# Optimization experiments

Hardware: AMD Instinct MI355X
Metric: run time of the kernel (lower is better)

## Reference

```python
import jax, jax.numpy as jnp
import numpy as np

B, N, F, FS, OUT, S, H, K = 1024, 256, 64, 128, 128, 4, 4, 4
EPS = 1e-5   # BatchNorm1d eps
BIG = 1e9    # sentinel distance for invalid nodes

# fully-connected segment edges (S nodes per graph, B graphs, flat node indexing)
_base = np.array([(i, j) for i in range(S) for j in range(S) if i != j], dtype=np.int32).T
_offs = (np.arange(B, dtype=np.int32) * S)[:, None]
CSRC = jnp.asarray((_base[0][None, :] + _offs).reshape(-1))
CDST = jnp.asarray((_base[1][None, :] + _offs).reshape(-1))
CMASK = jnp.ones(CSRC.shape[0], jnp.float32)


def _bn_relu(h, gamma, beta):
    # BatchNorm1d in training mode: biased batch statistics over the node axis
    mu = h.mean(0)
    var = jnp.var(h, axis=0)
    return jax.nn.relu((h - mu) * jax.lax.rsqrt(var + EPS) * gamma + beta)


def _graph_conv(x, src, dst, emask, W, b, gamma, beta):
    # linear -> gather(src) -> scatter-add(dst) -> degree norm -> BN -> ReLU
    h = x @ W + b
    agg = jax.ops.segment_sum(h[src] * emask[:, None], dst, num_segments=x.shape[0])
    deg = jnp.clip(jax.ops.segment_sum(emask, dst, num_segments=x.shape[0]), 1.0, None)
    return _bn_relu(h + agg / deg[:, None], gamma, beta)


def _knn_edges(positions, presence):
    # edges (i -> j) for each valid node i to its K nearest valid neighbors j
    valid = presence > 0.5                                    # [B,N]
    n_valid = valid.sum(-1)                                   # [B]
    diff = positions[:, :, None, :] - positions[:, None, :, :]
    d2 = jax.lax.stop_gradient(jnp.sum(diff * diff, -1))      # squared dist, same ordering as cdist
    d2 = jnp.where(valid[:, None, :], d2, BIG)                # mask invalid columns
    negv, idx = jax.lax.top_k(-d2, K + 1)                     # nearest first; idx[...,0] is self (dist 0)
    nbr, nd = idx[:, :, 1:], -negv[:, :, 1:]                  # [B,N,K]
    emask = valid[:, :, None] & (n_valid[:, None, None] >= 2) & (nd < 0.5 * BIG)
    offs = (jnp.arange(B) * N)[:, None, None]
    src = jnp.broadcast_to(jnp.arange(N)[None, :, None] + offs, (B, N, K)).reshape(-1)
    dst = jnp.where(emask, nbr + offs, 0).reshape(-1)
    return src, dst, emask.reshape(-1).astype(jnp.float32)


def setup_inputs() -> dict:
    key = jax.random.key(0)
    ks = jax.random.split(key, 16)
    rn = lambda k, shp, s=0.05: jax.random.normal(k, shp, jnp.float32) * s
    return {
        "axle_features": jax.random.normal(ks[0], (B, N, F), jnp.float32),
        "axle_positions": jax.random.normal(ks[1], (B, N, 2), jnp.float32),
        "presence_scores": jax.random.uniform(ks[2], (B, N), jnp.float32),
        "seg_queries": jax.random.normal(ks[3], (S, F), jnp.float32),
        "wq": rn(ks[4], (F, F)), "bq": jnp.zeros((F,), jnp.float32),
        "wk": rn(ks[5], (F, F)), "bk": jnp.zeros((F,), jnp.float32),
        "w_a2s": rn(ks[6], (F, FS)), "b_a2s": jnp.zeros((FS,), jnp.float32),
        "w_s2a": rn(ks[7], (FS, F)), "b_s2a": jnp.zeros((F,), jnp.float32),
        "coarse_W": rn(ks[8], (2, FS, FS)), "coarse_b": jnp.zeros((2, FS), jnp.float32),
        "coarse_gamma": jnp.ones((2, FS), jnp.float32), "coarse_beta": jnp.zeros((2, FS), jnp.float32),
        "fine_W": rn(ks[9], (3, F, F)), "fine_b": jnp.zeros((3, F), jnp.float32),
        "fine_gamma": jnp.ones((3, F), jnp.float32), "fine_beta": jnp.zeros((3, F), jnp.float32),
        "w_out": rn(ks[10], (F, OUT)), "b_out": jnp.zeros((OUT,), jnp.float32),
    }


def reference(axle_features, axle_positions, presence_scores, seg_queries, wq, bq, wk, bk,
              w_a2s, b_a2s, w_s2a, b_s2a, coarse_W, coarse_b, coarse_gamma, coarse_beta,
              fine_W, fine_b, fine_gamma, fine_beta, w_out, b_out):
    hd = F // H
    # LearnableSegmentation: MHA attention weights (head-averaged), then softmax over segments
    q = (seg_queries @ wq + bq).reshape(S, H, hd)
    k = (axle_features @ wk + bk).reshape(B, N, H, hd)
    scores = jnp.einsum('shd,bnhd->bhsn', q, k) / np.sqrt(hd)
    attn = jax.nn.softmax(scores, -1).mean(1)                 # [B,S,N]
    assign = jax.nn.softmax(jnp.swapaxes(attn, 1, 2), -1)     # [B,N,S]
    # segment pooling + coarse GNN over fully-connected segment graph
    proj = axle_features @ w_a2s + b_a2s                      # [B,N,FS]
    sf = jnp.einsum('bns,bnf->bsf', assign, proj).reshape(B * S, FS)
    for l in range(coarse_W.shape[0]):
        sf = _graph_conv(sf, CSRC, CDST, CMASK, coarse_W[l], coarse_b[l], coarse_gamma[l], coarse_beta[l])
    ctx = jnp.einsum('bns,bsf->bnf', assign, sf.reshape(B, S, FS)) @ w_s2a + b_s2a
    # fine GNN over kNN axle graph
    src, dst, em = _knn_edges(axle_positions, presence_scores)
    af = (axle_features + ctx).reshape(B * N, F)
    for l in range(fine_W.shape[0]):
        af = _graph_conv(af, src, dst, em, fine_W[l], fine_b[l], fine_gamma[l], fine_beta[l])
    # presence-weighted pooling + output projection
    pw = presence_scores[:, :, None]
    g = (af.reshape(B, N, F) * pw).sum(1) / jnp.clip(pw.sum(1), 1e-8, None)
    return g @ w_out + b_out
```

## Files before the change

### kernel.cpp

```cpp
#include <hip/hip_runtime.h>
#include <hip/hip_bf16.h>
#include <math.h>

#define BB   1024
#define NN   256
#define FF   64
#define FSS  128
#define OUTT 128
#define SS   4
#define HH   4
#define KK   4
#define HDD  16
#define EPSF 1e-5f
#define BIGF 1000000000.0f
#define ROWB 72
#define ROWA 68

typedef __attribute__((ext_vector_type(8))) short short8;
typedef __attribute__((ext_vector_type(4))) float f32x4;

static __device__ __forceinline__ unsigned short f2bf(float f) {
  union { float f; unsigned u; } x; x.f = f;
  unsigned u = x.u + 0x7fffu + ((x.u >> 16) & 1u);
  return (unsigned short)(u >> 16);
}
static __device__ __forceinline__ float bf2f(unsigned short h) {
  union { unsigned u; float f; } x; x.u = ((unsigned)h) << 16;
  return x.f;
}
static __device__ __forceinline__ float bflo(unsigned u) {
  union { unsigned u; float f; } x; x.u = u << 16; return x.f;
}
static __device__ __forceinline__ float bfhi(unsigned u) {
  union { unsigned u; float f; } x; x.u = u & 0xffff0000u; return x.f;
}
static __device__ __forceinline__ unsigned pack2(float a, float b) {
  return (unsigned)f2bf(a) | ((unsigned)f2bf(b) << 16);
}

__global__ __launch_bounds__(256) void k_prep(
    const float* __restrict__ sq, const float* __restrict__ wq, const float* __restrict__ bq,
    const float* __restrict__ wk, const float* __restrict__ bk,
    float* __restrict__ V_o, float* __restrict__ c_o)
{
  const int tid = threadIdx.x;
  __shared__ float sq_s[SS*FF];
  __shared__ float q_s[SS*FF];
  sq_s[tid] = sq[tid];
  __syncthreads();
  {
    int s = tid >> 6, f = tid & 63;
    float acc = bq[f];
    for (int c = 0; c < FF; ++c) acc += sq_s[s*FF+c] * wq[c*FF+f];
    q_s[s*FF+f] = acc;
  }
  __syncthreads();
  {
    int c = tid & 63, jb = (tid >> 6) * 4;
    for (int jj = 0; jj < 4; ++jj) {
      int j = jb + jj, h = j >> 2, s = j & 3;
      float acc = 0.f;
      for (int d = 0; d < HDD; ++d)
        acc += wk[c*FF + h*HDD + d] * q_s[s*FF + h*HDD + d];
      V_o[c*16 + j] = acc * 0.25f;
    }
  }
  if (tid < 16) {
    int h = tid >> 2, s = tid & 3;
    float acc = 0.f;
    for (int d = 0; d < HDD; ++d) acc += bk[h*HDD+d] * q_s[s*FF + h*HDD + d];
    c_o[tid] = acc * 0.25f;
  }
}

__global__ __launch_bounds__(256, 3) void k_attn_sf(
    const float* __restrict__ axle,
    const float* __restrict__ Vm, const float* __restrict__ cv,
    const float* __restrict__ w_a2s, const float* __restrict__ b_a2s,
    float* __restrict__ assign_o, float* __restrict__ sf_o)
{
  const int b = blockIdx.x, tid = threadIdx.x;
  const int wv = tid >> 6, ln = tid & 63;
  __shared__ __align__(16) unsigned short xb_a[NN*ROWA];
  __shared__ __align__(16) unsigned char u_buf[16*NN*2];
  __shared__ float mz_s[16][2];
  __hip_bfloat16* sc_s = (__hip_bfloat16*)u_buf;
  float (*as_s)[SS]    = (float (*)[SS])u_buf;
  float* t_s           = (float*)(u_buf + 4096);
  float* As_s          = (float*)(u_buf + 4096 + 1024);

  const float* afb = axle + (size_t)b*NN*FF;
  const float4* in4 = reinterpret_cast<const float4*>(afb);
  for (int i4 = tid; i4 < NN*FF/4; i4 += 256) {
    float4 v = in4[i4];
    int n = i4 >> 4, c4 = (i4 & 15) * 4;
    uint2 pk; pk.x = pack2(v.x, v.y); pk.y = pack2(v.z, v.w);
    *reinterpret_cast<uint2*>(&xb_a[n*ROWA + c4]) = pk;
  }
  __syncthreads();

  {
    float sc[16];
    #pragma unroll
    for (int j = 0; j < 16; ++j) sc[j] = cv[j];
    #pragma unroll
    for (int k = 0; k < 16; ++k) {
      uint2 pk = *reinterpret_cast<const uint2*>(&xb_a[tid*ROWA + 4*k]);
      float x0 = bflo(pk.x), x1 = bfhi(pk.x), x2 = bflo(pk.y), x3 = bfhi(pk.y);
      #pragma unroll
      for (int j = 0; j < 16; ++j) {
        float a = fmaf(x0, Vm[(4*k+0)*16+j], sc[j]);
        a = fmaf(x1, Vm[(4*k+1)*16+j], a);
        a = fmaf(x2, Vm[(4*k+2)*16+j], a);
        sc[j] = fmaf(x3, Vm[(4*k+3)*16+j], a);
      }
    }
    #pragma unroll
    for (int j = 0; j < 16; ++j) sc_s[j*NN + tid] = __float2bfloat16(sc[j]);
  }
  __syncthreads();

  for (int r = 0; r < 4; ++r) {
    int row = wv*4 + r;
    float v0 = __bfloat162float(sc_s[row*NN + ln]);
    float v1 = __bfloat162float(sc_s[row*NN + ln + 64]);
    float v2 = __bfloat162float(sc_s[row*NN + ln + 128]);
    float v3 = __bfloat162float(sc_s[row*NN + ln + 192]);
    float m = fmaxf(fmaxf(v0,v1), fmaxf(v2,v3));
    #pragma unroll
    for (int o = 32; o; o >>= 1) m = fmaxf(m, __shfl_xor(m, o));
    float z = __expf(v0-m) + __expf(v1-m) + __expf(v2-m) + __expf(v3-m);
    #pragma unroll
    for (int o = 32; o; o >>= 1) z += __shfl_xor(z, o);
    if (ln == 0) { mz_s[row][0] = m; mz_s[row][1] = 1.f/z; }
  }
  __syncthreads();

  float4 av;
  {
    float at0 = 0.f, at1 = 0.f, at2 = 0.f, at3 = 0.f;
    #pragma unroll
    for (int h = 0; h < HH; ++h) {
      at0 += __expf(__bfloat162float(sc_s[(h*4+0)*NN + tid]) - mz_s[h*4+0][0]) * mz_s[h*4+0][1];
      at1 += __expf(__bfloat162float(sc_s[(h*4+1)*NN + tid]) - mz_s[h*4+1][0]) * mz_s[h*4+1][1];
      at2 += __expf(__bfloat162float(sc_s[(h*4+2)*NN + tid]) - mz_s[h*4+2][0]) * mz_s[h*4+2][1];
      at3 += __expf(__bfloat162float(sc_s[(h*4+3)*NN + tid]) - mz_s[h*4+3][0]) * mz_s[h*4+3][1];
    }
    at0 *= 0.25f; at1 *= 0.25f; at2 *= 0.25f; at3 *= 0.25f;
    float m = fmaxf(fmaxf(at0,at1), fmaxf(at2,at3));
    float e0=__expf(at0-m), e1=__expf(at1-m), e2=__expf(at2-m), e3=__expf(at3-m);
    float zi = 1.f/(e0+e1+e2+e3);
    av = make_float4(e0*zi, e1*zi, e2*zi, e3*zi);
    reinterpret_cast<float4*>(assign_o)[(size_t)b*NN + tid] = av;
  }
  __syncthreads();
  *reinterpret_cast<float4*>(&as_s[tid][0]) = av;
  __syncthreads();

  {
    int s = wv, half = ln >> 5, c2 = ln & 31;
    float t0 = 0.f, t1 = 0.f, aa = 0.f;
    int n0 = half * 128;
    for (int n = n0; n < n0 + 128; ++n) {
      float a = as_s[n][s];
      unsigned pk = *reinterpret_cast<const unsigned*>(&xb_a[n*ROWA + 2*c2]);
      t0 = fmaf(a, bflo(pk), t0);
      t1 = fmaf(a, bfhi(pk), t1);
      aa += a;
    }
    t0 += __shfl_xor(t0, 32);
    t1 += __shfl_xor(t1, 32);
    aa += __shfl_xor(aa, 32);
    if (half == 0) {
      t_s[s*FF + 2*c2]     = t0;
      t_s[s*FF + 2*c2 + 1] = t1;
      if (c2 == 0) As_s[s] = aa;
    }
  }
  __syncthreads();

  for (int o = tid; o < SS*FSS; o += 256) {
    int s = o >> 7, f = o & 127;
    float acc = As_s[s] * b_a2s[f];
    for (int c = 0; c < FF; ++c) acc += t_s[s*FF + c] * w_a2s[c*FSS+f];
    sf_o[((size_t)b*SS+s)*FSS+f] = acc;
  }
}

__global__ __launch_bounds__(128) void k_coarse(
    const float* __restrict__ in, const float* __restrict__ W, const float* __restrict__ bias,
    const float* __restrict__ pmu, const float* __restrict__ prstd,
    const float* __restrict__ pgamma, const float* __restrict__ pbeta, int applyBN,
    float* __restrict__ out, float* __restrict__ stat1, float* __restrict__ stat2)
{
  const int b = blockIdx.x, f = threadIdx.x;
  __shared__ float x_s[SS][FSS];
  #pragma unroll
  for (int i = 0; i < SS; ++i) {
    float v = in[((size_t)b*SS+i)*FSS + f];
    if (applyBN) v = fmaxf((v - pmu[f])*prstd[f]*pgamma[f] + pbeta[f], 0.f);
    x_s[i][f] = v;
  }
  __syncthreads();
  float h0 = bias[f], h1 = h0, h2 = h0, h3 = h0;
  for (int c = 0; c < FSS; ++c) {
    float w = W[c*FSS+f];
    h0 += x_s[0][c]*w; h1 += x_s[1][c]*w; h2 += x_s[2][c]*w; h3 += x_s[3][c]*w;
  }
  float s4 = h0+h1+h2+h3;
  const float inv3 = 1.f/3.f;
  float o0 = h0 + (s4-h0)*inv3;
  float o1 = h1 + (s4-h1)*inv3;
  float o2 = h2 + (s4-h2)*inv3;
  float o3 = h3 + (s4-h3)*inv3;
  size_t ob = (size_t)b*SS*FSS + f;
  out[ob] = o0; out[ob+FSS] = o1; out[ob+2*FSS] = o2; out[ob+3*FSS] = o3;
  stat1[(size_t)f*BB + b] = o0+o1+o2+o3;
  stat2[(size_t)f*BB + b] = o0*o0+o1*o1+o2*o2+o3*o3;
}

__global__ __launch_bounds__(256) void k_bnstats(
    const float* __restrict__ s1, const float* __restrict__ s2,
    float* __restrict__ mu, float* __restrict__ rstd, float invcnt)
{
  const int f = blockIdx.x, tid = threadIdx.x;
  float a = 0.f, q = 0.f;
  for (int j = tid; j < BB; j += 256) { a += s1[(size_t)f*BB+j]; q += s2[(size_t)f*BB+j]; }
  #pragma unroll
  for (int o = 32; o; o >>= 1) { a += __shfl_xor(a, o); q += __shfl_xor(q, o); }
  __shared__ float ra[4], rq[4];
  int wv = tid >> 6;
  if ((tid & 63) == 0) { ra[wv] = a; rq[wv] = q; }
  __syncthreads();
  if (tid == 0) {
    float s = ra[0]+ra[1]+ra[2]+ra[3], ss = rq[0]+rq[1]+rq[2]+rq[3];
    float m = s*invcnt; float v = ss*invcnt - m*m;
    mu[f] = m; rstd[f] = 1.f / sqrtf(v + EPSF);
  }
}

__global__ __launch_bounds__(512) void k_knn(
    const float* __restrict__ pos, const float* __restrict__ pres,
    int* __restrict__ rev_go, int* __restrict__ offs_go,
    float* __restrict__ ivd_o)
{
  const int b = blockIdx.x, tid = threadIdx.x;
  const int ln = tid & 63, wv = tid >> 6;
  const int n = tid >> 1, half = tid & 1;
  __shared__ float2 pp[NN];
  __shared__ int vld[NN];
  __shared__ int wcnt[4];
  __shared__ int nbr_s[NN*KK];
  __shared__ int cnti[NN], scn[NN], cur[NN];
  __shared__ __align__(16) int rev_s[NN*KK];

  if (tid < NN) {
    float2 p = reinterpret_cast<const float2*>(pos)[(size_t)b*NN + tid];
    float pr = pres[(size_t)b*NN + tid];
    int v = pr > 0.5f ? 1 : 0;
    vld[tid] = v;
    pp[tid] = v ? p : make_float2(3.4e38f, 3.4e38f);
    cnti[tid] = 0; cur[tid] = 0;
    reinterpret_cast<int4*>(rev_s)[tid] = make_int4(0,0,0,0);
    int cnt = v;
    #pragma unroll
    for (int o = 32; o; o >>= 1) cnt += __shfl_xor(cnt, o);
    if (ln == 0) wcnt[wv] = cnt;
  }
  __syncthreads();
  const int nv = wcnt[0]+wcnt[1]+wcnt[2]+wcnt[3];

  float2 sp = pp[n];
  const float xi = sp.x, yi = sp.y;
  float b0=3.4e38f, b1=b0, b2=b0, b3=b0, b4=b0;
  int   j0=0, j1=0, j2=0, j3=0, j4=0;
  const int jb = half << 7;
  for (int j = jb; j < jb + 128; ++j) {
    float2 q = pp[j];
    float dx = __fsub_rn(xi, q.x);
    float dy = __fsub_rn(yi, q.y);
    float d2 = __fadd_rn(__fmul_rn(dx,dx), __fmul_rn(dy,dy));
    if (d2 < b4) {
      b4 = d2; j4 = j;
      if (b4 < b3) { float t=b3; b3=b4; b4=t; int ti=j3; j3=j4; j4=ti; }
      if (b3 < b2) { float t=b2; b2=b3; b3=t; int ti=j2; j2=j3; j3=ti; }
      if (b2 < b1) { float t=b1; b1=b2; b2=t; int ti=j1; j1=j2; j2=ti; }
      if (b1 < b0) { float t=b0; b0=b1; b1=t; int ti=j0; j0=j1; j1=ti; }
    }
  }
  float c0 = __shfl_xor(b0,1), c1 = __shfl_xor(b1,1), c2 = __shfl_xor(b2,1),
        c3 = __shfl_xor(b3,1), c4 = __shfl_xor(b4,1);
  int   k0 = __shfl_xor(j0,1), k1 = __shfl_xor(j1,1), k2 = __shfl_xor(j2,1),
        k3 = __shfl_xor(j3,1), k4 = __shfl_xor(j4,1);

  if (half == 0) {
#define MSTEP(OD, OJ) do { bool ta = (b0 <= c0); \
    OD = ta ? b0 : c0; OJ = ta ? j0 : k0; \
    b0 = ta ? b1 : b0; j0 = ta ? j1 : j0; \
    b1 = ta ? b2 : b1; j1 = ta ? j2 : j1; \
    b2 = ta ? b3 : b2; j2 = ta ? j3 : j2; \
    b3 = ta ? b4 : b3; j3 = ta ? j4 : j3; \
    b4 = ta ? 3.4e38f : b4; \
    c0 = ta ? c0 : c1; k0 = ta ? k0 : k1; \
    c1 = ta ? c1 : c2; k1 = ta ? k1 : k2; \
    c2 = ta ? c2 : c3; k2 = ta ? k2 : k3; \
    c3 = ta ? c3 : c4; k3 = ta ? k3 : k4; \
    c4 = ta ? c4 : 3.4e38f; } while(0)
    float m0d, dd1, dd2, dd3, dd4; int m0j, i1, i2, i3, i4;
    MSTEP(m0d, m0j);
    MSTEP(dd1, i1); MSTEP(dd2, i2); MSTEP(dd3, i3); MSTEP(dd4, i4);
#undef MSTEP
    (void)m0d; (void)m0j;
    bool okrow = (vld[n] != 0) && (nv >= 2);
    int e0 = (okrow && dd1 < 0.5f*BIGF) ? i1 : -1;
    int e1 = (okrow && dd2 < 0.5f*BIGF) ? i2 : -1;
    int e2 = (okrow && dd3 < 0.5f*BIGF) ? i3 : -1;
    int e3 = (okrow && dd4 < 0.5f*BIGF) ? i4 : -1;
    nbr_s[n*KK+0] = e0; nbr_s[n*KK+1] = e1;
    nbr_s[n*KK+2] = e2; nbr_s[n*KK+3] = e3;
    if (e0 >= 0) atomicAdd(&cnti[e0], 1);
    if (e1 >= 0) atomicAdd(&cnti[e1], 1);
    if (e2 >= 0) atomicAdd(&cnti[e2], 1);
    if (e3 >= 0) atomicAdd(&cnti[e3], 1);
  }
  __syncthreads();

  if (tid < NN) scn[tid] = cnti[tid];
  __syncthreads();
  for (int d = 1; d < NN; d <<= 1) {
    int t = 0;
    if (tid < NN && tid >= d) t = scn[tid-d];
    __syncthreads();
    if (tid < NN) scn[tid] += t;
    __syncthreads();
  }
  if (tid < NN) {
    #pragma unroll
    for (int k = 0; k < KK; ++k) {
      int d = nbr_s[tid*KK+k];
      if (d >= 0) {
        int pp2 = atomicAdd(&cur[d], 1);
        rev_s[scn[d] - cnti[d] + pp2] = tid;
      }
    }
  }
  __syncthreads();

  if (tid < NN) {
    int start = scn[tid] - cnti[tid];
    offs_go[(size_t)b*(NN+1) + tid] = start;
    if (tid == NN-1) offs_go[(size_t)b*(NN+1) + NN] = scn[NN-1];
    int cnt = cnti[tid];
    float r = 1.f / fmaxf((float)cnt, 1.f);
    ivd_o[(size_t)b*NN + tid] = cnt > 0 ? -r : r;
    reinterpret_cast<int4*>(rev_go)[(size_t)b*NN + tid] =
        *reinterpret_cast<int4*>(&rev_s[tid*KK]);
  }
}

__global__ __launch_bounds__(256) void k_ctx(
    const float* __restrict__ axle, const float* __restrict__ hc1,
    const float* __restrict__ mu, const float* __restrict__ rstd,
    const float* __restrict__ gamma, const float* __restrict__ beta,
    const float* __restrict__ assign_i,
    const float* __restrict__ w_s2a, const float* __restrict__ b_s2a,
    unsigned short* __restrict__ af_o)
{
  const int b = blockIdx.x, tid = threadIdx.x;
  __shared__ float csf[SS][FSS];
  __shared__ float u_s[SS][FF];
  for (int i = tid; i < SS*FSS; i += 256) {
    int s = i >> 7, f = i & 127;
    float v = hc1[((size_t)b*SS+s)*FSS + f];
    csf[s][f] = fmaxf((v - mu[f])*rstd[f]*gamma[f] + beta[f], 0.f);
  }
  __syncthreads();
  {
    int s = tid >> 6, f = tid & 63;
    float acc = 0.f;
    for (int c = 0; c < FSS; ++c) acc += csf[s][c] * w_s2a[c*FF+f];
    u_s[s][f] = acc;
  }
  __syncthreads();
  const size_t gb = (size_t)b*NN*FF;
  const float4* ax4 = reinterpret_cast<const float4*>(axle + gb);
  uint2* out2 = reinterpret_cast<uint2*>(af_o + gb);
  for (int i4 = tid; i4 < NN*FF/4; i4 += 256) {
    int n = i4 >> 4, c4 = (i4 & 15) * 4;
    float4 ax = ax4[i4];
    float4 ag = reinterpret_cast<const float4*>(assign_i)[(size_t)b*NN + n];
    float o0 = ax.x + b_s2a[c4+0] + ag.x*u_s[0][c4+0] + ag.y*u_s[1][c4+0] + ag.z*u_s[2][c4+0] + ag.w*u_s[3][c4+0];
    float o1 = ax.y + b_s2a[c4+1] + ag.x*u_s[0][c4+1] + ag.y*u_s[1][c4+1] + ag.z*u_s[2][c4+1] + ag.w*u_s[3][c4+1];
    float o2 = ax.z + b_s2a[c4+2] + ag.x*u_s[0][c4+2] + ag.y*u_s[1][c4+2] + ag.z*u_s[2][c4+2] + ag.w*u_s[3][c4+2];
    float o3 = ax.w + b_s2a[c4+3] + ag.x*u_s[0][c4+3] + ag.y*u_s[1][c4+3] + ag.z*u_s[2][c4+3] + ag.w*u_s[3][c4+3];
    uint2 pk; pk.x = pack2(o0, o1); pk.y = pack2(o2, o3);
    out2[i4] = pk;
  }
}

__global__ __launch_bounds__(512, 4) void k_fine3(
    unsigned short* __restrict__ af,
    const float* __restrict__ W, const float* __restrict__ bias,
    const float* __restrict__ pmu, const float* __restrict__ prstd,
    const float* __restrict__ pgamma, const float* __restrict__ pbeta, int applyBN,
    const int* __restrict__ rev_g, const int* __restrict__ offs_g,
    const float* __restrict__ ivd_g,
    float* __restrict__ stat1, float* __restrict__ stat2)
{
  const int b = blockIdx.x, tid = threadIdx.x;
  const int wv = tid >> 6, ln = tid & 63;
  const int l15 = ln & 15, g = ln >> 4;
  __shared__ __align__(16) unsigned short xb[NN*ROWB];
  __shared__ __align__(16) unsigned short wt[FF*ROWB];
  __shared__ __align__(16) int rev_s[NN*KK];
  __shared__ unsigned short offs_s[NN+1];
  __shared__ float ivd_s[NN];
  __shared__ float scale_s[FF], shift_s[FF];
  float* red1 = (float*)rev_s;
  float* red2 = red1 + 8*FF;

  if (tid < FF) {
    if (applyBN) {
      float sc = prstd[tid]*pgamma[tid];
      scale_s[tid] = sc; shift_s[tid] = pbeta[tid] - pmu[tid]*sc;
    } else { scale_s[tid] = 1.f; shift_s[tid] = 0.f; }
  }
  for (int i = tid; i < NN*KK; i += 512) rev_s[i] = rev_g[(size_t)b*NN*KK + i];
  if (tid <= NN) offs_s[tid] = (unsigned short)offs_g[(size_t)b*(NN+1) + tid];
  if (tid < NN) ivd_s[tid] = ivd_g[(size_t)b*NN + tid];

  {
    const int c = tid >> 3, f0 = (tid & 7) * 8;
    float4 w0 = *reinterpret_cast<const float4*>(&W[c*FF + f0]);
    float4 w1 = *reinterpret_cast<const float4*>(&W[c*FF + f0 + 4]);
    wt[(f0+0)*ROWB + c] = f2bf(w0.x);
    wt[(f0+1)*ROWB + c] = f2bf(w0.y);
    wt[(f0+2)*ROWB + c] = f2bf(w0.z);
    wt[(f0+3)*ROWB + c] = f2bf(w0.w);
    wt[(f0+4)*ROWB + c] = f2bf(w1.x);
    wt[(f0+5)*ROWB + c] = f2bf(w1.y);
    wt[(f0+6)*ROWB + c] = f2bf(w1.z);
    wt[(f0+7)*ROWB + c] = f2bf(w1.w);
  }

  unsigned short* afb = af + (size_t)b*NN*FF;
  const uint4* in8 = reinterpret_cast<const uint4*>(afb);
  __syncthreads();

  for (int i8 = tid; i8 < NN*FF/8; i8 += 512) {
    uint4 raw = in8[i8];
    int n = i8 >> 3, c8 = (i8 & 7) * 8;
    float v0 = bflo(raw.x), v1 = bfhi(raw.x), v2 = bflo(raw.y), v3 = bfhi(raw.y);
    float v4 = bflo(raw.z), v5 = bfhi(raw.z), v6 = bflo(raw.w), v7 = bfhi(raw.w);
    v0 = v0*scale_s[c8+0] + shift_s[c8+0];
    v1 = v1*scale_s[c8+1] + shift_s[c8+1];
    v2 = v2*scale_s[c8+2] + shift_s[c8+2];
    v3 = v3*scale_s[c8+3] + shift_s[c8+3];
    v4 = v4*scale_s[c8+4] + shift_s[c8+4];
    v5 = v5*scale_s[c8+5] + shift_s[c8+5];
    v6 = v6*scale_s[c8+6] + shift_s[c8+6];
    v7 = v7*scale_s[c8+7] + shift_s[c8+7];
    if (applyBN) {
      v0=fmaxf(v0,0.f); v1=fmaxf(v1,0.f); v2=fmaxf(v2,0.f); v3=fmaxf(v3,0.f);
      v4=fmaxf(v4,0.f); v5=fmaxf(v5,0.f); v6=fmaxf(v6,0.f); v7=fmaxf(v7,0.f);
    }
    uint4 pk;
    pk.x = pack2(v0, v1); pk.y = pack2(v2, v3);
    pk.z = pack2(v4, v5); pk.w = pack2(v6, v7);
    *reinterpret_cast<uint4*>(&xb[n*ROWB + c8]) = pk;
  }
  __syncthreads();

  const int nb = wv << 5;
#define GATH(J) float y##J; { const int n_ = nb + (J); \
    const int s0_ = offs_s[n_]; const int s1_ = offs_s[n_+1]; \
    float sum_ = 0.f; \
    for (int i_ = s0_; i_ < s1_; ++i_) sum_ += bf2f(xb[rev_s[i_]*ROWB + ln]); \
    y##J = bf2f(xb[n_*ROWB + ln]) + fabsf(ivd_s[n_])*sum_; }
  GATH(0)  GATH(1)  GATH(2)  GATH(3)  GATH(4)  GATH(5)  GATH(6)  GATH(7)
  GATH(8)  GATH(9)  GATH(10) GATH(11) GATH(12) GATH(13) GATH(14) GATH(15)
  GATH(16) GATH(17) GATH(18) GATH(19) GATH(20) GATH(21) GATH(22) GATH(23)
  GATH(24) GATH(25) GATH(26) GATH(27) GATH(28) GATH(29) GATH(30) GATH(31)
#undef GATH
  __syncthreads();
#define WRB(J) xb[(nb + (J))*ROWB + ln] = f2bf(y##J);
  WRB(0)  WRB(1)  WRB(2)  WRB(3)  WRB(4)  WRB(5)  WRB(6)  WRB(7)
  WRB(8)  WRB(9)  WRB(10) WRB(11) WRB(12) WRB(13) WRB(14) WRB(15)
  WRB(16) WRB(17) WRB(18) WRB(19) WRB(20) WRB(21) WRB(22) WRB(23)
  WRB(24) WRB(25) WRB(26) WRB(27) WRB(28) WRB(29) WRB(30) WRB(31)
#undef WRB
  __syncthreads();

  short8 areg[2][2], breg[4][2];
  #pragma unroll
  for (int rt2 = 0; rt2 < 2; ++rt2)
    #pragma unroll
    for (int ks = 0; ks < 2; ++ks)
      areg[rt2][ks] = *reinterpret_cast<const short8*>(
          &xb[((2*wv+rt2)*16 + l15)*ROWB + ks*32 + g*8]);
  #pragma unroll
  for (int ct = 0; ct < 4; ++ct)
    #pragma unroll
    for (int ks = 0; ks < 2; ++ks)
      breg[ct][ks] = *reinterpret_cast<const short8*>(
          &wt[(ct*16 + l15)*ROWB + ks*32 + g*8]);

  f32x4 acc[2][4];
  #pragma unroll
  for (int rt2 = 0; rt2 < 2; ++rt2)
    #pragma unroll
    for (int ct = 0; ct < 4; ++ct)
      acc[rt2][ct] = (f32x4){0.f, 0.f, 0.f, 0.f};
  #pragma unroll
  for (int rt2 = 0; rt2 < 2; ++rt2)
    #pragma unroll
    for (int ct = 0; ct < 4; ++ct)
      #pragma unroll
      for (int ks = 0; ks < 2; ++ks)
        acc[rt2][ct] = __builtin_amdgcn_mfma_f32_16x16x32_bf16(
            areg[rt2][ks], breg[ct][ks], acc[rt2][ct], 0, 0, 0);

  float bias_c[4];
  #pragma unroll
  for (int ct = 0; ct < 4; ++ct) bias_c[ct] = bias[ct*16 + l15];
  float ps[4] = {0.f,0.f,0.f,0.f}, pss[4] = {0.f,0.f,0.f,0.f};
  #pragma unroll
  for (int rt2 = 0; rt2 < 2; ++rt2) {
    #pragma unroll
    for (int i = 0; i < 4; ++i) {
      int row = (2*wv+rt2)*16 + g*4 + i;
      float bfr = ivd_s[row] < 0.f ? 2.f : 1.f;
      #pragma unroll
      for (int ct = 0; ct < 4; ++ct) {
        float o = acc[rt2][ct][i] + bfr*bias_c[ct];
        xb[row*ROWB + ct*16 + l15] = f2bf(o);
        ps[ct] += o; pss[ct] += o*o;
      }
    }
  }
  #pragma unroll
  for (int ct = 0; ct < 4; ++ct) {
    float p = ps[ct], q = pss[ct];
    p += __shfl_xor(p, 16); p += __shfl_xor(p, 32);
    q += __shfl_xor(q, 16); q += __shfl_xor(q, 32);
    if (g == 0) { red1[wv*FF + ct*16 + l15] = p; red2[wv*FF + ct*16 + l15] = q; }
  }
  __syncthreads();

  uint4* out8 = reinterpret_cast<uint4*>(afb);
  for (int i8 = tid; i8 < NN*FF/8; i8 += 512) {
    int n = i8 >> 3, c8 = (i8 & 7) * 8;
    out8[i8] = *reinterpret_cast<const uint4*>(&xb[n*ROWB + c8]);
  }
  if (tid < FF) {
    float s = 0.f, ss = 0.f;
    #pragma unroll
    for (int w = 0; w < 8; ++w) { s += red1[w*FF + tid]; ss += red2[w*FF + tid]; }
    stat1[(size_t)tid*BB + b] = s;
    stat2[(size_t)tid*BB + b] = ss;
  }
}

__global__ __launch_bounds__(256) void k_pool(
    const unsigned short* __restrict__ af, const float* __restrict__ pres,
    const float* __restrict__ pmu, const float* __restrict__ prstd,
    const float* __restrict__ pgamma, const float* __restrict__ pbeta,
    const float* __restrict__ w_out, const float* __restrict__ b_out,
    float* __restrict__ out)
{
  const int b = blockIdx.x, tid = threadIdx.x;
  const int wv = tid >> 6, ln = tid & 63;
  __shared__ float pr_s2[NN];
  __shared__ float red[FF][9];
  __shared__ float g_s[FF];
  __shared__ float prsum_s[4];
  float pw = pres[(size_t)b*NN + tid];
  pr_s2[tid] = pw;
  float t = pw;
  #pragma unroll
  for (int o = 32; o; o >>= 1) t += __shfl_xor(t, o);
  if (ln == 0) prsum_s[wv] = t;
  __syncthreads();

  const int c2 = (tid & 31) * 2, jrow = tid >> 5;
  float sc0 = prstd[c2+0]*pgamma[c2+0], sh0 = pbeta[c2+0] - pmu[c2+0]*sc0;
  float sc1 = prstd[c2+1]*pgamma[c2+1], sh1 = pbeta[c2+1] - pmu[c2+1]*sc1;
  float s0 = 0.f, s1 = 0.f;
  const unsigned* af2 = reinterpret_cast<const unsigned*>(af + (size_t)b*NN*FF);
  for (int n = jrow; n < NN; n += 8) {
    unsigned pk = af2[n*(FF/2) + (tid & 31)];
    float p = pr_s2[n];
    s0 += fmaxf(bflo(pk)*sc0 + sh0, 0.f) * p;
    s1 += fmaxf(bfhi(pk)*sc1 + sh1, 0.f) * p;
  }
  red[c2+0][jrow] = s0;
  red[c2+1][jrow] = s1;
  __syncthreads();
  if (tid < FF) {
    float s = 0.f;
    #pragma unroll
    for (int j = 0; j < 8; ++j) s += red[tid][j];
    float den = fmaxf(prsum_s[0]+prsum_s[1]+prsum_s[2]+prsum_s[3], 1e-8f);
    g_s[tid] = s / den;
  }
  __syncthreads();
  if (tid < OUTT) {
    float acc = b_out[tid];
    for (int f = 0; f < FF; ++f) acc += g_s[f] * w_out[f*OUTT + tid];
    out[(size_t)b*OUTT + tid] = acc;
  }
}

extern "C" void kernel_launch(void* const* d_in, const int* in_sizes, int n_in,
                              void* d_out, int out_size, void* d_ws, size_t ws_size,
                              hipStream_t stream) {
  (void)in_sizes; (void)n_in; (void)out_size; (void)ws_size;
  const float* axle  = (const float*)d_in[0];
  const float* pos   = (const float*)d_in[1];
  const float* pres  = (const float*)d_in[2];
  const float* sq    = (const float*)d_in[3];
  const float* wq    = (const float*)d_in[4];
  const float* bq    = (const float*)d_in[5];
  const float* wk    = (const float*)d_in[6];
  const float* bk    = (const float*)d_in[7];
  const float* w_a2s = (const float*)d_in[8];
  const float* b_a2s = (const float*)d_in[9];
  const float* w_s2a = (const float*)d_in[10];
  const float* b_s2a = (const float*)d_in[11];
  const float* cW    = (const float*)d_in[12];
  const float* cb    = (const float*)d_in[13];
  const float* cg    = (const float*)d_in[14];
  const float* cbe   = (const float*)d_in[15];
  const float* fW    = (const float*)d_in[16];
  const float* fb    = (const float*)d_in[17];
  const float* fg    = (const float*)d_in[18];
  const float* fbe   = (const float*)d_in[19];
  const float* wout  = (const float*)d_in[20];
  const float* bout  = (const float*)d_in[21];
  float* out = (float*)d_out;

  char* base = (char*)d_ws;
  size_t off = 0;
  auto alloc = [&](size_t nbytes) -> void* {
    void* p = base + off; off += (nbytes + 255) & ~(size_t)255; return p;
  };
  unsigned short* af = (unsigned short*)alloc((size_t)BB*NN*FF*2);
  float* assign = (float*)alloc((size_t)BB*NN*SS*4);
  float* sf     = (float*)alloc((size_t)BB*SS*FSS*4);
  float* hc0    = (float*)alloc((size_t)BB*SS*FSS*4);
  float* hc1    = (float*)alloc((size_t)BB*SS*FSS*4);
  int*   rev    = (int*)  alloc((size_t)BB*NN*KK*4);
  int*   offs   = (int*)  alloc((size_t)BB*(NN+1)*4);
  float* ivd    = (float*)alloc((size_t)BB*NN*4);
  float* st1    = (float*)alloc((size_t)FSS*BB*4);
  float* st2    = (float*)alloc((size_t)FSS*BB*4);
  float* mu0    = (float*)alloc(FSS*4);
  float* rs0    = (float*)alloc(FSS*4);
  float* mu1    = (float*)alloc(FSS*4);
  float* rs1    = (float*)alloc(FSS*4);
  float* muF    = (float*)alloc(FF*4);
  float* rsF    = (float*)alloc(FF*4);
  float* Vm     = (float*)alloc(FF*16*4);
  float* cv     = (float*)alloc(16*4);

  k_prep<<<1, 256, 0, stream>>>(sq, wq, bq, wk, bk, Vm, cv);
  k_attn_sf<<<BB, 256, 0, stream>>>(axle, Vm, cv, w_a2s, b_a2s, assign, sf);

  k_coarse<<<BB, 128, 0, stream>>>(sf,  cW,          cb,     mu0, rs0, cg, cbe, 0, hc0, st1, st2);
  k_bnstats<<<FSS, 256, 0, stream>>>(st1, st2, mu0, rs0, 1.f/((float)BB*SS));
  k_coarse<<<BB, 128, 0, stream>>>(hc0, cW+FSS*FSS,  cb+FSS, mu0, rs0, cg, cbe, 1, hc1, st1, st2);
  k_bnstats<<<FSS, 256, 0, stream>>>(st1, st2, mu1, rs1, 1.f/((float)BB*SS));

  k_knn<<<BB, 512, 0, stream>>>(pos, pres, rev, offs, ivd);

  k_ctx<<<BB, 256, 0, stream>>>(axle, hc1, mu1, rs1, cg+FSS, cbe+FSS, assign, w_s2a, b_s2a, af);

  k_fine3<<<BB, 512, 0, stream>>>(af, fW,         fb,      muF, rsF, fg,    fbe,    0, rev, offs, ivd, st1, st2);
  k_bnstats<<<FF, 256, 0, stream>>>(st1, st2, muF, rsF, 1.f/((float)BB*NN));
  k_fine3<<<BB, 512, 0, stream>>>(af, fW+FF*FF,   fb+FF,   muF, rsF, fg,    fbe,    1, rev, offs, ivd, st1, st2);
  k_bnstats<<<FF, 256, 0, stream>>>(st1, st2, muF, rsF, 1.f/((float)BB*NN));
  k_fine3<<<BB, 512, 0, stream>>>(af, fW+2*FF*FF, fb+2*FF, muF, rsF, fg+FF, fbe+FF, 1, rev, offs, ivd, st1, st2);
  k_bnstats<<<FF, 256, 0, stream>>>(st1, st2, muF, rsF, 1.f/((float)BB*NN));

  k_pool<<<BB, 256, 0, stream>>>(af, pres, muF, rsF, fg+2*FF, fbe+2*FF, wout, bout, out);
}
```

Measured before the change: 281.5 us.

## Replace BN stats kernels with atomic accumulation and fold finalize into consumers

Removes the five separate k_bnstats reduction launches. Producers now atomically add per-feature sum and sum-of-squares into a small zeroed stats buffer, and each consumer kernel derives mean and rstd itself. This also widens k_ctx to 512 threads. It cuts launch overhead and the per-graph stat arrays, at the cost of 1024-way atomic contention per feature and a nondeterministic float summation order.

Result: slower. 340.9 us (+21.1%).

```diff
diff --git a/kernel.cpp b/kernel.cpp
--- a/kernel.cpp
+++ b/kernel.cpp
@@ -15,6 +15,7 @@
 #define BIGF 1000000000.0f
 #define ROWB 72
 #define ROWA 68
+#define STT  256
 
 typedef __attribute__((ext_vector_type(8))) short short8;
 typedef __attribute__((ext_vector_type(4))) float f32x4;
@@ -41,11 +42,12 @@
 __global__ __launch_bounds__(256) void k_prep(
     const float* __restrict__ sq, const float* __restrict__ wq, const float* __restrict__ bq,
     const float* __restrict__ wk, const float* __restrict__ bk,
-    float* __restrict__ V_o, float* __restrict__ c_o)
+    float* __restrict__ V_o, float* __restrict__ c_o, float* __restrict__ stats_all)
 {
   const int tid = threadIdx.x;
   __shared__ float sq_s[SS*FF];
   __shared__ float q_s[SS*FF];
+  for (int i = tid; i < 5*STT; i += 256) stats_all[i] = 0.f;
   sq_s[tid] = sq[tid];
   __syncthreads();
   {
@@ -189,16 +191,23 @@
 
 __global__ __launch_bounds__(128) void k_coarse(
     const float* __restrict__ in, const float* __restrict__ W, const float* __restrict__ bias,
-    const float* __restrict__ pmu, const float* __restrict__ prstd,
+    const float* __restrict__ stats_in, float invcnt,
     const float* __restrict__ pgamma, const float* __restrict__ pbeta, int applyBN,
-    float* __restrict__ out, float* __restrict__ stat1, float* __restrict__ stat2)
+    float* __restrict__ out, float* __restrict__ stats_out)
 {
   const int b = blockIdx.x, f = threadIdx.x;
   __shared__ float x_s[SS][FSS];
+  float sc = 1.f, sh = 0.f;
+  if (applyBN) {
+    float m = stats_in[f] * invcnt;
+    float var = stats_in[128+f] * invcnt - m*m;
+    float rstd = 1.f / sqrtf(var + EPSF);
+    sc = rstd * pgamma[f]; sh = pbeta[f] - m*sc;
+  }
   #pragma unroll
   for (int i = 0; i < SS; ++i) {
     float v = in[((size_t)b*SS+i)*FSS + f];
-    if (applyBN) v = fmaxf((v - pmu[f])*prstd[f]*pgamma[f] + pbeta[f], 0.f);
+    if (applyBN) v = fmaxf(v*sc + sh, 0.f);
     x_s[i][f] = v;
   }
   __syncthreads();
@@ -215,28 +224,8 @@
   float o3 = h3 + (s4-h3)*inv3;
   size_t ob = (size_t)b*SS*FSS + f;
   out[ob] = o0; out[ob+FSS] = o1; out[ob+2*FSS] = o2; out[ob+3*FSS] = o3;
-  stat1[(size_t)f*BB + b] = o0+o1+o2+o3;
-  stat2[(size_t)f*BB + b] = o0*o0+o1*o1+o2*o2+o3*o3;
-}
-
-__global__ __launch_bounds__(256) void k_bnstats(
-    const float* __restrict__ s1, const float* __restrict__ s2,
-    float* __restrict__ mu, float* __restrict__ rstd, float invcnt)
-{
-  const int f = blockIdx.x, tid = threadIdx.x;
-  float a = 0.f, q = 0.f;
-  for (int j = tid; j < BB; j += 256) { a += s1[(size_t)f*BB+j]; q += s2[(size_t)f*BB+j]; }
-  #pragma unroll
-  for (int o = 32; o; o >>= 1) { a += __shfl_xor(a, o); q += __shfl_xor(q, o); }
-  __shared__ float ra[4], rq[4];
-  int wv = tid >> 6;
-  if ((tid & 63) == 0) { ra[wv] = a; rq[wv] = q; }
-  __syncthreads();
-  if (tid == 0) {
-    float s = ra[0]+ra[1]+ra[2]+ra[3], ss = rq[0]+rq[1]+rq[2]+rq[3];
-    float m = s*invcnt; float v = ss*invcnt - m*m;
-    mu[f] = m; rstd[f] = 1.f / sqrtf(v + EPSF);
-  }
+  atomicAdd(&stats_out[f],     o0+o1+o2+o3);
+  atomicAdd(&stats_out[128+f], o0*o0+o1*o1+o2*o2+o3*o3);
 }
 
 __global__ __launch_bounds__(512) void k_knn(
@@ -358,9 +347,9 @@
   }
 }
 
-__global__ __launch_bounds__(256) void k_ctx(
+__global__ __launch_bounds__(512) void k_ctx2(
     const float* __restrict__ axle, const float* __restrict__ hc1,
-    const float* __restrict__ mu, const float* __restrict__ rstd,
+    const float* __restrict__ stats_in, float invcnt,
     const float* __restrict__ gamma, const float* __restrict__ beta,
     const float* __restrict__ assign_i,
     const float* __restrict__ w_s2a, const float* __restrict__ b_s2a,
@@ -369,13 +358,22 @@
   const int b = blockIdx.x, tid = threadIdx.x;
   __shared__ float csf[SS][FSS];
   __shared__ float u_s[SS][FF];
-  for (int i = tid; i < SS*FSS; i += 256) {
-    int s = i >> 7, f = i & 127;
+  __shared__ float sc2_s[FSS], sh2_s[FSS];
+  if (tid < FSS) {
+    float m = stats_in[tid] * invcnt;
+    float var = stats_in[128+tid] * invcnt - m*m;
+    float rstd = 1.f / sqrtf(var + EPSF);
+    float sc = rstd * gamma[tid];
+    sc2_s[tid] = sc; sh2_s[tid] = beta[tid] - m*sc;
+  }
+  __syncthreads();
+  {
+    int s = tid >> 7, f = tid & 127;
     float v = hc1[((size_t)b*SS+s)*FSS + f];
-    csf[s][f] = fmaxf((v - mu[f])*rstd[f]*gamma[f] + beta[f], 0.f);
-  }
-  __syncthreads();
-  {
+    csf[s][f] = fmaxf(v*sc2_s[f] + sh2_s[f], 0.f);
+  }
+  __syncthreads();
+  if (tid < 256) {
     int s = tid >> 6, f = tid & 63;
     float acc = 0.f;
     for (int c = 0; c < FSS; ++c) acc += csf[s][c] * w_s2a[c*FF+f];
@@ -385,7 +383,7 @@
   const size_t gb = (size_t)b*NN*FF;
   const float4* ax4 = reinterpret_cast<const float4*>(axle + gb);
   uint2* out2 = reinterpret_cast<uint2*>(af_o + gb);
-  for (int i4 = tid; i4 < NN*FF/4; i4 += 256) {
+  for (int i4 = tid; i4 < NN*FF/4; i4 += 512) {
     int n = i4 >> 4, c4 = (i4 & 15) * 4;
     float4 ax = ax4[i4];
     float4 ag = reinterpret_cast<const float4*>(assign_i)[(size_t)b*NN + n];
@@ -401,11 +399,11 @@
 __global__ __launch_bounds__(512, 4) void k_fine3(
     unsigned short* __restrict__ af,
     const float* __restrict__ W, const float* __restrict__ bias,
-    const float* __restrict__ pmu, const float* __restrict__ prstd,
+    const float* __restrict__ stats_in, float invcnt,
     const float* __restrict__ pgamma, const float* __restrict__ pbeta, int applyBN,
     const int* __restrict__ rev_g, const int* __restrict__ offs_g,
     const float* __restrict__ ivd_g,
-    float* __restrict__ stat1, float* __restrict__ stat2)
+    float* __restrict__ stats_out)
 {
   const int b = blockIdx.x, tid = threadIdx.x;
   const int wv = tid >> 6, ln = tid & 63;
@@ -421,8 +419,11 @@
 
   if (tid < FF) {
     if (applyBN) {
-      float sc = prstd[tid]*pgamma[tid];
-      scale_s[tid] = sc; shift_s[tid] = pbeta[tid] - pmu[tid]*sc;
+      float m = stats_in[tid] * invcnt;
+      float var = stats_in[128+tid] * invcnt - m*m;
+      float rstd = 1.f / sqrtf(var + EPSF);
+      float sc = rstd * pgamma[tid];
+      scale_s[tid] = sc; shift_s[tid] = pbeta[tid] - m*sc;
     } else { scale_s[tid] = 1.f; shift_s[tid] = 0.f; }
   }
   for (int i = tid; i < NN*KK; i += 512) rev_s[i] = rev_g[(size_t)b*NN*KK + i];
@@ -556,14 +557,14 @@
     float s = 0.f, ss = 0.f;
     #pragma unroll
     for (int w = 0; w < 8; ++w) { s += red1[w*FF + tid]; ss += red2[w*FF + tid]; }
-    stat1[(size_t)tid*BB + b] = s;
-    stat2[(size_t)tid*BB + b] = ss;
+    atomicAdd(&stats_out[tid],     s);
+    atomicAdd(&stats_out[128+tid], ss);
   }
 }
 
 __global__ __launch_bounds__(256) void k_pool(
     const unsigned short* __restrict__ af, const float* __restrict__ pres,
-    const float* __restrict__ pmu, const float* __restrict__ prstd,
+    const float* __restrict__ stats_in, float invcnt,
     const float* __restrict__ pgamma, const float* __restrict__ pbeta,
     const float* __restrict__ w_out, const float* __restrict__ b_out,
     float* __restrict__ out)
@@ -583,8 +584,12 @@
   __syncthreads();
 
   const int c2 = (tid & 31) * 2, jrow = tid >> 5;
-  float sc0 = prstd[c2+0]*pgamma[c2+0], sh0 = pbeta[c2+0] - pmu[c2+0]*sc0;
-  float sc1 = prstd[c2+1]*pgamma[c2+1], sh1 = pbeta[c2+1] - pmu[c2+1]*sc1;
+  float m0 = stats_in[c2+0]*invcnt, m1 = stats_in[c2+1]*invcnt;
+  float va0 = stats_in[128+c2+0]*invcnt - m0*m0;
+  float va1 = stats_in[128+c2+1]*invcnt - m1*m1;
+  float r0 = 1.f/sqrtf(va0+EPSF), r1 = 1.f/sqrtf(va1+EPSF);
+  float sc0 = r0*pgamma[c2+0], sh0 = pbeta[c2+0] - m0*sc0;
+  float sc1 = r1*pgamma[c2+1], sh1 = pbeta[c2+1] - m1*sc1;
   float s0 = 0.f, s1 = 0.f;
   const unsigned* af2 = reinterpret_cast<const unsigned*>(af + (size_t)b*NN*FF);
   for (int n = jrow; n < NN; n += 8) {
@@ -652,35 +657,27 @@
   int*   rev    = (int*)  alloc((size_t)BB*NN*KK*4);
   int*   offs   = (int*)  alloc((size_t)BB*(NN+1)*4);
   float* ivd    = (float*)alloc((size_t)BB*NN*4);
-  float* st1    = (float*)alloc((size_t)FSS*BB*4);
-  float* st2    = (float*)alloc((size_t)FSS*BB*4);
-  float* mu0    = (float*)alloc(FSS*4);
-  float* rs0    = (float*)alloc(FSS*4);
-  float* mu1    = (float*)alloc(FSS*4);
-  float* rs1    = (float*)alloc(FSS*4);
-  float* muF    = (float*)alloc(FF*4);
-  float* rsF    = (float*)alloc(FF*4);
+  float* stats  = (float*)alloc(5*STT*4);
   float* Vm     = (float*)alloc(FF*16*4);
   float* cv     = (float*)alloc(16*4);
-
-  k_prep<<<1, 256, 0, stream>>>(sq, wq, bq, wk, bk, Vm, cv);
+  float* stA = stats, *stB = stats+STT, *stC = stats+2*STT, *stD = stats+3*STT, *stE = stats+4*STT;
+
+  const float inv_c = 1.f/((float)BB*SS);
+  const float inv_f = 1.f/((float)BB*NN);
+
+  k_prep<<<1, 256, 0, stream>>>(sq, wq, bq, wk, bk, Vm, cv, stats);
   k_attn_sf<<<BB, 256, 0, stream>>>(axle, Vm, cv, w_a2s, b_a2s, assign, sf);
 
-  k_coarse<<<BB, 128, 0, stream>>>(sf,  cW,          cb,     mu0, rs0, cg, cbe, 0, hc0, st1, st2);
-  k_bnstats<<<FSS, 256, 0, stream>>>(st1, st2, mu0, rs0, 1.f/((float)BB*SS));
-  k_coarse<<<BB, 128, 0, stream>>>(hc0, cW+FSS*FSS,  cb+FSS, mu0, rs0, cg, cbe, 1, hc1, st1, st2);
-  k_bnstats<<<FSS, 256, 0, stream>>>(st1, st2, mu1, rs1, 1.f/((float)BB*SS));
+  k_coarse<<<BB, 128, 0, stream>>>(sf,  cW,         cb,     stats, 0.f,   cg, cbe, 0, hc0, stA);
+  k_coarse<<<BB, 128, 0, stream>>>(hc0, cW+FSS*FSS, cb+FSS, stA,   inv_c, cg, cbe, 1, hc1, stB);
 
   k_knn<<<BB, 512, 0, stream>>>(pos, pres, rev, offs, ivd);
-
-  k_ctx<<<BB, 256, 0, stream>>>(axle, hc1, mu1, rs1, cg+FSS, cbe+FSS, assign, w_s2a, b_s2a, af);
-
-  k_fine3<<<BB, 512, 0, stream>>>(af, fW,         fb,      muF, rsF, fg,    fbe,    0, rev, offs, ivd, st1, st2);
-  k_bnstats<<<FF, 256, 0, stream>>>(st1, st2, muF, rsF, 1.f/((float)BB*NN));
-  k_fine3<<<BB, 512, 0, stream>>>(af, fW+FF*FF,   fb+FF,   muF, rsF, fg,    fbe,    1, rev, offs, ivd, st1, st2);
-  k_bnstats<<<FF, 256, 0, stream>>>(st1, st2, muF, rsF, 1.f/((float)BB*NN));
-  k_fine3<<<BB, 512, 0, stream>>>(af, fW+2*FF*FF, fb+2*FF, muF, rsF, fg+FF, fbe+FF, 1, rev, offs, ivd, st1, st2);
-  k_bnstats<<<FF, 256, 0, stream>>>(st1, st2, muF, rsF, 1.f/((float)BB*NN));
-
-  k_pool<<<BB, 256, 0, stream>>>(af, pres, muF, rsF, fg+2*FF, fbe+2*FF, wout, bout, out);
-}
+  k_ctx2<<<BB, 512, 0, stream>>>(axle, hc1, stB, inv_c, cg+FSS, cbe+FSS,
+                                 assign, w_s2a, b_s2a, af);
+
+  k_fine3<<<BB, 512, 0, stream>>>(af, fW,         fb,      stats, 0.f,   fg,    fbe,    0, rev, offs, ivd, stC);
+  k_fine3<<<BB, 512, 0, stream>>>(af, fW+FF*FF,   fb+FF,   stC,   inv_f, fg,    fbe,    1, rev, offs, ivd, stD);
+  k_fine3<<<BB, 512, 0, stream>>>(af, fW+2*FF*FF, fb+2*FF, stD,   inv_f, fg+FF, fbe+FF, 1, rev, offs, ivd, stE);
+
+  k_pool<<<BB, 256, 0, stream>>>(af, pres, stE, inv_f, fg+2*FF, fbe+2*FF, wout, bout, out);
+}
```
